# Performance work log

Measured on AMD Instinct MI355X. Metric: run time of the kernel, lower is better.

## Reference

```python
import jax, jax.numpy as jnp
import numpy as np

B, C, H, W = 2, 256, 64, 64
D = 4  # max dilation ring


def _offsets():
    offs = [(0, 0)]
    for s in range(1, D + 1):
        for a in (-s, 0, s):
            for b in (-s, 0, s):
                if a != 0 or b != 0:
                    offs.append((a, b))
    return np.array(offs, dtype=np.int32)  # (33, 2)


def setup_inputs() -> dict:
    key = jax.random.key(0)
    k1, k2, k3, k4 = jax.random.split(key, 4)
    scale = 1.0 / np.sqrt(C)
    return {
        "Ft": jax.random.normal(k1, (B, C, H, W), dtype=jnp.float32),
        "Ft_epsilon": jax.random.normal(k2, (B, C, H, W), dtype=jnp.float32),
        "Wf": jax.random.normal(k3, (256, C), dtype=jnp.float32) * scale,
        "bf": jnp.zeros((256,), dtype=jnp.float32),
        "Wg": jax.random.normal(k4, (256, C), dtype=jnp.float32) * scale,
        "bg": jnp.zeros((256,), dtype=jnp.float32),
    }


def reference(Ft, Ft_epsilon, Wf, bf, Wg, bg):
    # 1x1 conv embeddings
    Ef = jnp.einsum("bchw,oc->bohw", Ft, Wf) + bf[None, :, None, None]          # f(Ft)
    Eg = jnp.einsum("bchw,oc->bohw", Ft_epsilon, Wg) + bg[None, :, None, None]  # g(Ft_eps)

    offs = _offsets()                                  # (K,2), K=33
    dx = jnp.asarray(offs[:, 0])[:, None, None]        # (K,1,1)
    dy = jnp.asarray(offs[:, 1])[:, None, None]
    xs = jnp.arange(H)[None, :, None] + dx             # (K,H,1)
    ys = jnp.arange(W)[None, None, :] + dy             # (K,1,W)
    valid = ((xs >= 0) & (xs < H)) & ((ys >= 0) & (ys < W))  # (K,H,W)
    xc = jnp.clip(xs, 0, H - 1)
    yc = jnp.clip(ys, 0, W - 1)

    # gather neighbor embeddings and features: (B,C,K,H,W)
    Ef_n = Ef[:, :, xc, yc]
    Ft_n = Ft[:, :, xc, yc]

    # affinity of center embedding with each neighbor embedding
    aff = jnp.einsum("bchw,bckhw->bkhw", Eg, Ef_n)     # (B,K,H,W)
    aff = jnp.where(valid[None], aff, -jnp.inf)        # clip out-of-bounds neighbors
    w = jax.nn.softmax(aff, axis=1)                    # (B,K,H,W); center always valid

    out = jnp.einsum("bkhw,bckhw->bchw", w, Ft_n)      # (B,C,H,W)
    return out
```

## Files before the change

kernel.cpp:

```cpp
#include <hip/hip_runtime.h>
#include <math.h>

typedef __attribute__((ext_vector_type(4))) float f4;

__device__ __forceinline__ int iclamp(int x, int lo, int hi) { return min(max(x, lo), hi); }

__device__ constexpr int DXC[33] = {0, -1,-1,-1,0,0,1,1,1, -2,-2,-2,0,0,2,2,2, -3,-3,-3,0,0,3,3,3, -4,-4,-4,0,0,4,4,4};
__device__ constexpr int DYC[33] = {0, -1,0,1,-1,1,-1,0,1, -2,0,2,-2,2,-2,0,2, -3,0,3,-3,3,-3,0,3, -4,0,4,-4,4,-4,0,4};

__global__ __launch_bounds__(256) void mat_M(
    const float* __restrict__ Wf, const float* __restrict__ Wg,
    const float* __restrict__ bg, float* __restrict__ Mt, float* __restrict__ r)
{
    __shared__ float Sf[32][33], Sg[32][33];
    __shared__ float Rs[32][9];
    const int c1b = blockIdx.x * 32, c2b = blockIdx.y * 32;
    const int tid = threadIdx.x;
    const int tx = tid & 15, ty = tid >> 4;
    float acc[2][2] = {};
    for (int ko = 0; ko < 256; ko += 32) {
        #pragma unroll
        for (int i = 0; i < 4; ++i) {
            int f = i * 256 + tid, o = f >> 5, c = f & 31;
            Sf[o][c] = Wf[(ko + o) * 256 + c1b + c];
            Sg[o][c] = Wg[(ko + o) * 256 + c2b + c];
        }
        __syncthreads();
        #pragma unroll
        for (int o = 0; o < 32; ++o) {
            float f0 = Sf[o][ty * 2], f1 = Sf[o][ty * 2 + 1];
            float g0 = Sg[o][tx * 2], g1 = Sg[o][tx * 2 + 1];
            acc[0][0] += f0 * g0; acc[0][1] += f0 * g1;
            acc[1][0] += f1 * g0; acc[1][1] += f1 * g1;
        }
        __syncthreads();
    }
    #pragma unroll
    for (int i = 0; i < 2; ++i)
        #pragma unroll
        for (int j = 0; j < 2; ++j)
            Mt[(size_t)(c2b + tx * 2 + j) * 256 + c1b + ty * 2 + i] = acc[i][j];

    if (blockIdx.y == 0) {
        const int c1l = tid & 31, og = tid >> 5;
        float s = 0.f;
        #pragma unroll 8
        for (int o = og * 32; o < og * 32 + 32; ++o)
            s += Wf[o * 256 + c1b + c1l] * bg[o];
        Rs[c1l][og] = s;
        __syncthreads();
        if (tid < 32) {
            float t = 0.f;
            #pragma unroll
            for (int j = 0; j < 8; ++j) t += Rs[tid][j];
            r[c1b + tid] = t;
        }
    }
}

template<bool LO, bool HI>
__device__ __forceinline__ void ldwin(float* wn, const float* Lb, int rd, int ch, int wq) {
    const float* p = &Lb[(rd * 8 + ch) * 72 + wq * 4];
    if constexpr (LO) { f4 v = *(const f4*)p;       wn[0]=v.x; wn[1]=v.y; wn[2]=v.z;  wn[3]=v.w; }
    {                   f4 v = *(const f4*)(p + 4); wn[4]=v.x; wn[5]=v.y; wn[6]=v.z;  wn[7]=v.w; }
    if constexpr (HI) { f4 v = *(const f4*)(p + 8); wn[8]=v.x; wn[9]=v.y; wn[10]=v.z; wn[11]=v.w; }
}

template<int DY>
__device__ __forceinline__ void fmadd4(f4& a, const f4& eg, const float* wn) {
    a.x += eg.x * wn[4 + DY];
    a.y += eg.y * wn[5 + DY];
    a.z += eg.z * wn[6 + DY];
    a.w += eg.w * wn[7 + DY];
}

template<int KQ>
__device__ __forceinline__ void aff_compute(const float* Lb, const float* egb,
                                            int wq, int cg, f4* acc)
{
    #pragma unroll
    for (int chi = 0; chi < 2; ++chi) {
        const int ch = cg * 2 + chi;
        f4 eg = *(const f4*)&egb[ch * 68 + wq * 4];
        float wn[12];
        if constexpr (KQ == 0) {
            ldwin<true,true>(wn, Lb, 0, ch, wq);
            fmadd4<-4>(acc[0], eg, wn); fmadd4<0>(acc[1], eg, wn); fmadd4<4>(acc[2], eg, wn);
            ldwin<true,true>(wn, Lb, 1, ch, wq);
            fmadd4<-3>(acc[3], eg, wn); fmadd4<0>(acc[4], eg, wn); fmadd4<3>(acc[5], eg, wn);
            ldwin<true,true>(wn, Lb, 2, ch, wq);
            fmadd4<-2>(acc[6], eg, wn); fmadd4<0>(acc[7], eg, wn); fmadd4<2>(acc[8], eg, wn);
        } else if constexpr (KQ == 1) {
            ldwin<true,true>(wn, Lb, 3, ch, wq);
            fmadd4<-1>(acc[0], eg, wn); fmadd4<0>(acc[1], eg, wn); fmadd4<1>(acc[2], eg, wn);
            ldwin<true,false>(wn, Lb, 4, ch, wq);
            fmadd4<-1>(acc[3], eg, wn); fmadd4<-2>(acc[4], eg, wn);
            fmadd4<-3>(acc[5], eg, wn); fmadd4<-4>(acc[6], eg, wn);
        } else if constexpr (KQ == 2) {
            ldwin<false,true>(wn, Lb, 4, ch, wq);
            fmadd4<0>(acc[0], eg, wn); fmadd4<1>(acc[1], eg, wn); fmadd4<2>(acc[2], eg, wn);
            fmadd4<3>(acc[3], eg, wn); fmadd4<4>(acc[4], eg, wn);
            ldwin<true,true>(wn, Lb, 5, ch, wq);
            fmadd4<-1>(acc[5], eg, wn); fmadd4<0>(acc[6], eg, wn); fmadd4<1>(acc[7], eg, wn);
        } else {
            ldwin<true,true>(wn, Lb, 6, ch, wq);
            fmadd4<-2>(acc[0], eg, wn); fmadd4<0>(acc[1], eg, wn); fmadd4<2>(acc[2], eg, wn);
            ldwin<true,true>(wn, Lb, 7, ch, wq);
            fmadd4<-3>(acc[3], eg, wn); fmadd4<0>(acc[4], eg, wn); fmadd4<3>(acc[5], eg, wn);
            ldwin<true,true>(wn, Lb, 8, ch, wq);
            fmadd4<-4>(acc[6], eg, wn); fmadd4<0>(acc[7], eg, wn); fmadd4<4>(acc[8], eg, wn);
        }
    }
}

__global__ __launch_bounds__(256, 2) void gemm_aff(
    const float* __restrict__ Mt, const float* __restrict__ rw,
    const float* __restrict__ FtE, const float* __restrict__ Ftg,
    float* __restrict__ part)
{
    __shared__ float SH[16384];
    const int h = blockIdx.x, b = blockIdx.y, cseg = blockIdx.z;
    const int tid = threadIdx.x;

    float* Gs = SH;
    float* L0 = SH + 4352;

    {
        float* Ms = SH;
        const int tn = tid & 15, tm = tid >> 4;
        const int m0 = cseg * 64;
        const float* X = FtE + (size_t)b * 1048576 + h * 64 + tn * 4;

        #pragma unroll
        for (int i = 0; i < 16; ++i) {
            int f = i * 256 + tid;
            int k = f >> 4, mi = f & 15;
            *(f4*)&Ms[k * 64 + mi * 4] = *(const f4*)&Mt[(size_t)k * 256 + m0 + mi * 4];
        }
        __syncthreads();

        f4 acc0 = {0.f,0.f,0.f,0.f}, acc1 = acc0, acc2 = acc0, acc3 = acc0;
        for (int kc = 0; kc < 256; kc += 8) {
            f4 x0 = *(const f4*)(X + (size_t)(kc + 0) * 4096);
            f4 x1 = *(const f4*)(X + (size_t)(kc + 1) * 4096);
            f4 x2 = *(const f4*)(X + (size_t)(kc + 2) * 4096);
            f4 x3 = *(const f4*)(X + (size_t)(kc + 3) * 4096);
            f4 x4 = *(const f4*)(X + (size_t)(kc + 4) * 4096);
            f4 x5 = *(const f4*)(X + (size_t)(kc + 5) * 4096);
            f4 x6 = *(const f4*)(X + (size_t)(kc + 6) * 4096);
            f4 x7 = *(const f4*)(X + (size_t)(kc + 7) * 4096);
            f4 a0 = *(const f4*)&Ms[(kc + 0) * 64 + tm * 4];
            f4 a1 = *(const f4*)&Ms[(kc + 1) * 64 + tm * 4];
            f4 a2 = *(const f4*)&Ms[(kc + 2) * 64 + tm * 4];
            f4 a3 = *(const f4*)&Ms[(kc + 3) * 64 + tm * 4];
            f4 a4 = *(const f4*)&Ms[(kc + 4) * 64 + tm * 4];
            f4 a5 = *(const f4*)&Ms[(kc + 5) * 64 + tm * 4];
            f4 a6 = *(const f4*)&Ms[(kc + 6) * 64 + tm * 4];
            f4 a7 = *(const f4*)&Ms[(kc + 7) * 64 + tm * 4];
            acc0 += x0 * a0.x; acc1 += x0 * a0.y; acc2 += x0 * a0.z; acc3 += x0 * a0.w;
            acc0 += x1 * a1.x; acc1 += x1 * a1.y; acc2 += x1 * a1.z; acc3 += x1 * a1.w;
            acc0 += x2 * a2.x; acc1 += x2 * a2.y; acc2 += x2 * a2.z; acc3 += x2 * a2.w;
            acc0 += x3 * a3.x; acc1 += x3 * a3.y; acc2 += x3 * a3.z; acc3 += x3 * a3.w;
            acc0 += x4 * a4.x; acc1 += x4 * a4.y; acc2 += x4 * a4.z; acc3 += x4 * a4.w;
            acc0 += x5 * a5.x; acc1 += x5 * a5.y; acc2 += x5 * a5.z; acc3 += x5 * a5.w;
            acc0 += x6 * a6.x; acc1 += x6 * a6.y; acc2 += x6 * a6.z; acc3 += x6 * a6.w;
            acc0 += x7 * a7.x; acc1 += x7 * a7.y; acc2 += x7 * a7.z; acc3 += x7 * a7.w;
        }
        __syncthreads();

        const int m0g = m0 + tm * 4;
        f4 v;
        v = acc0 + rw[m0g + 0]; *(f4*)&Gs[(tm * 4 + 0) * 68 + tn * 4] = v;
        v = acc1 + rw[m0g + 1]; *(f4*)&Gs[(tm * 4 + 1) * 68 + tn * 4] = v;
        v = acc2 + rw[m0g + 2]; *(f4*)&Gs[(tm * 4 + 2) * 68 + tn * 4] = v;
        v = acc3 + rw[m0g + 3]; *(f4*)&Gs[(tm * 4 + 3) * 68 + tn * 4] = v;
    }

    const int wq = tid & 15, cg = (tid >> 4) & 3, kq = tid >> 6;
    const float* FtB = Ftg + (size_t)b * 1048576;
    const int cbase = cseg * 64;

    int hr[9];
    #pragma unroll
    for (int d = 0; d < 9; ++d) hr[d] = iclamp(h + d - 4, 0, 63);

    f4 vreg[5]; float sreg[3];

    auto load_rnd = [&](int rr) {
        const int c0 = cbase + rr * 8;
        #pragma unroll
        for (int i = 0; i < 5; ++i) {
            int f = i * 256 + tid;
            if (f < 1152) {
                int d = f >> 7, rem = f & 127, ch = rem >> 4, c4 = rem & 15;
                vreg[i] = *(const f4*)&FtB[(size_t)(c0 + ch) * 4096 + hr[d] * 64 + c4 * 4];
            }
        }
        #pragma unroll
        for (int i = 0; i < 3; ++i) {
            int e = i * 256 + tid;
            if (e < 576) {
                int row = e >> 3, sc = e & 7, d = row >> 3, ch = row & 7;
                int wsrc = (sc < 4) ? 0 : 63;
                sreg[i] = FtB[(size_t)(c0 + ch) * 4096 + hr[d] * 64 + wsrc];
            }
        }
    };
    auto store_rnd = [&](int buf) {
        float* Lb = L0 + buf * 5184;
        #pragma unroll
        for (int i = 0; i < 5; ++i) {
            int f = i * 256 + tid;
            if (f < 1152) {
                int d = f >> 7, rem = f & 127, ch = rem >> 4, c4 = rem & 15;
                *(f4*)&Lb[(d * 8 + ch) * 72 + 4 + c4 * 4] = vreg[i];
            }
        }
        #pragma unroll
        for (int i = 0; i < 3; ++i) {
            int e = i * 256 + tid;
            if (e < 576) {
                int row = e >> 3, sc = e & 7, d = row >> 3, ch = row & 7;
                int col = (sc < 4) ? sc : (64 + sc);
                Lb[(d * 8 + ch) * 72 + col] = sreg[i];
            }
        }
    };

    f4 acc[9] = {};

    load_rnd(0); store_rnd(0);
    for (int rr = 0; rr < 8; ++rr) {
        if (rr < 7) load_rnd(rr + 1);
        __syncthreads();
        const float* Lb = L0 + (rr & 1) * 5184;
        const float* egb = Gs + rr * 8 * 68;
        switch (kq) {
            case 0: aff_compute<0>(Lb, egb, wq, cg, acc); break;
            case 1: aff_compute<1>(Lb, egb, wq, cg, acc); break;
            case 2: aff_compute<2>(Lb, egb, wq, cg, acc); break;
            default: aff_compute<3>(Lb, egb, wq, cg, acc); break;
        }
        if (rr < 7) store_rnd((rr + 1) & 1);
    }

    #pragma unroll
    for (int j = 0; j < 9; ++j) {
        acc[j].x += __shfl_xor(acc[j].x, 16); acc[j].x += __shfl_xor(acc[j].x, 32);
        acc[j].y += __shfl_xor(acc[j].y, 16); acc[j].y += __shfl_xor(acc[j].y, 32);
        acc[j].z += __shfl_xor(acc[j].z, 16); acc[j].z += __shfl_xor(acc[j].z, 32);
        acc[j].w += __shfl_xor(acc[j].w, 16); acc[j].w += __shfl_xor(acc[j].w, 32);
    }

    if (cg == 0) {
        float* pB = part + (((size_t)cseg * 2 + b) * 33) * 4096 + h * 64 + wq * 4;
        #define STP(K, J) *(f4*)&pB[(size_t)(K) * 4096] = acc[J];
        switch (kq) {
            case 0: STP(25,0) STP(26,1) STP(27,2) STP(17,3) STP(18,4) STP(19,5) STP(9,6) STP(10,7) STP(11,8) break;
            case 1: STP(1,0) STP(2,1) STP(3,2) STP(4,3) STP(12,4) STP(20,5) STP(28,6) break;
            case 2: STP(0,0) STP(5,1) STP(13,2) STP(21,3) STP(29,4) STP(6,5) STP(7,6) STP(8,7) break;
            default: STP(14,0) STP(15,1) STP(16,2) STP(22,3) STP(23,4) STP(24,5) STP(30,6) STP(31,7) STP(32,8) break;
        }
        #undef STP
    }
}

__global__ __launch_bounds__(256, 2) void out_kernel(
    const float* __restrict__ part, const float* __restrict__ Ft,
    float* __restrict__ out)
{
    __shared__ float L[2][9 * 8 * 72];

    const int h = blockIdx.x, b = blockIdx.y, cseg = blockIdx.z;
    const int tid = threadIdx.x;
    const int w = tid & 63, cg = tid >> 6;
    const size_t plane = (size_t)b * 256 * 4096;
    const float* FtB = Ft + plane;
    float* outB = out + plane;
    const int cbase = cseg * 64;
    const int p = h * 64 + w;

    int hr[9];
    #pragma unroll
    for (int d = 0; d < 9; ++d) hr[d] = iclamp(h + d - 4, 0, 63);

    f4 vreg[5]; float sreg[3];

    auto load_rnd = [&](int rr) {
        const int c0 = cbase + rr * 8;
        #pragma unroll
        for (int i = 0; i < 5; ++i) {
            int f = i * 256 + tid;
            if (f < 1152) {
                int d = f >> 7, rem = f & 127, ch = rem >> 4, c4 = rem & 15;
                vreg[i] = *(const f4*)&FtB[(size_t)(c0 + ch) * 4096 + hr[d] * 64 + c4 * 4];
            }
        }
        #pragma unroll
        for (int i = 0; i < 3; ++i) {
            int e = i * 256 + tid;
            if (e < 576) {
                int row = e >> 3, sc = e & 7, d = row >> 3, ch = row & 7;
                int wsrc = (sc < 4) ? 0 : 63;
                sreg[i] = FtB[(size_t)(c0 + ch) * 4096 + hr[d] * 64 + wsrc];
            }
        }
    };
    auto store_rnd = [&](int buf) {
        float* Lb = L[buf];
        #pragma unroll
        for (int i = 0; i < 5; ++i) {
            int f = i * 256 + tid;
            if (f < 1152) {
                int d = f >> 7, rem = f & 127, ch = rem >> 4, c4 = rem & 15;
                *(f4*)&Lb[(d * 8 + ch) * 72 + 4 + c4 * 4] = vreg[i];
            }
        }
        #pragma unroll
        for (int i = 0; i < 3; ++i) {
            int e = i * 256 + tid;
            if (e < 576) {
                int row = e >> 3, sc = e & 7, d = row >> 3, ch = row & 7;
                int col = (sc < 4) ? sc : (64 + sc);
                Lb[(d * 8 + ch) * 72 + col] = sreg[i];
            }
        }
    };

    load_rnd(0);

    float wv[33];
    {
        constexpr size_t CS = (size_t)2 * 33 * 4096;
        const float* pB = part + ((size_t)b * 33) * 4096 + p;
        float mx = -INFINITY;
        #pragma unroll
        for (int k = 0; k < 33; ++k) {
            size_t off = (size_t)k * 4096;
            float s = pB[off] + pB[CS + off] + pB[2 * CS + off] + pB[3 * CS + off];
            bool valid = ((unsigned)(h + DXC[k]) < 64u) && ((unsigned)(w + DYC[k]) < 64u);
            wv[k] = valid ? s : -INFINITY;
            mx = fmaxf(mx, wv[k]);
        }
        float ssum = 0.f;
        #pragma unroll
        for (int k = 0; k < 33; ++k) { float e = __expf(wv[k] - mx); wv[k] = e; ssum += e; }
        float inv = 1.0f / ssum;
        #pragma unroll
        for (int k = 0; k < 33; ++k) wv[k] *= inv;
    }

    store_rnd(0);
    for (int rr = 0; rr < 8; ++rr) {
        if (rr < 7) load_rnd(rr + 1);
        __syncthreads();
        const float* base = &L[rr & 1][4 + w];
        #pragma unroll
        for (int u = 0; u < 2; ++u) {
            const float* b2 = base + (cg * 2 + u) * 72;
            float o = 0.f;
            #pragma unroll
            for (int k = 0; k < 33; ++k)
                o += wv[k] * b2[(DXC[k] + 4) * 576 + DYC[k]];
            int c = cbase + rr * 8 + cg * 2 + u;
            outB[(size_t)c * 4096 + p] = o;
        }
        if (rr < 7) store_rnd((rr + 1) & 1);
    }
}

extern "C" void kernel_launch(void* const* d_in, const int* in_sizes, int n_in,
                              void* d_out, int out_size, void* d_ws, size_t ws_size,
                              hipStream_t stream) {
    const float* Ft  = (const float*)d_in[0];
    const float* FtE = (const float*)d_in[1];
    const float* Wf  = (const float*)d_in[2];
    const float* bf  = (const float*)d_in[3];
    const float* Wg  = (const float*)d_in[4];
    const float* bg  = (const float*)d_in[5];
    float* out = (float*)d_out;
    (void)bf;

    float* part = (float*)d_ws;
    float* Mt   = part + (size_t)4 * 2 * 33 * 4096;
    float* rw   = Mt + 256 * 256;

    hipLaunchKernelGGL(mat_M,      dim3(8, 8),     dim3(256), 0, stream, Wf, Wg, bg, Mt, rw);
    hipLaunchKernelGGL(gemm_aff,   dim3(64, 2, 4), dim3(256), 0, stream, Mt, rw, FtE, Ft, part);
    hipLaunchKernelGGL(out_kernel, dim3(64, 2, 4), dim3(256), 0, stream, part, Ft, out);
}
```

Baseline: 141.2 us.

## Split out_kernel neighbor sum across offset groups with vectorized window loads

The output aggregation is restructured so each thread handles four adjacent pixels and one quarter of the 33 offsets (grouped by row), reusing a loaded 12-wide LDS window across several offsets. Softmax weights are staged through shared memory and redistributed per offset group. The four partial sums are reduced through an extra shared buffer, then stored with float4 writes. This cuts LDS reads per FMA but adds a __syncthreads, extra shared memory, and only half the threads do the final reduction and store.

```diff
diff --git a/kernel.cpp b/kernel.cpp
--- a/kernel.cpp
+++ b/kernel.cpp
@@ -265,15 +265,60 @@
     }
 }
 
+template<int KQ>
+__device__ __forceinline__ void out_compute(const float* Lb, const f4* wv,
+                                            int wq, int ch0, f4* acc)
+{
+    #pragma unroll
+    for (int chi = 0; chi < 2; ++chi) {
+        const int ch = ch0 + chi;
+        f4& a = acc[chi];
+        float wn[12];
+        if constexpr (KQ == 0) {
+            ldwin<true,true>(wn, Lb, 0, ch, wq);
+            fmadd4<-4>(a, wv[0], wn); fmadd4<0>(a, wv[1], wn); fmadd4<4>(a, wv[2], wn);
+            ldwin<true,true>(wn, Lb, 1, ch, wq);
+            fmadd4<-3>(a, wv[3], wn); fmadd4<0>(a, wv[4], wn); fmadd4<3>(a, wv[5], wn);
+            ldwin<true,true>(wn, Lb, 2, ch, wq);
+            fmadd4<-2>(a, wv[6], wn); fmadd4<0>(a, wv[7], wn); fmadd4<2>(a, wv[8], wn);
+        } else if constexpr (KQ == 1) {
+            ldwin<true,true>(wn, Lb, 3, ch, wq);
+            fmadd4<-1>(a, wv[0], wn); fmadd4<0>(a, wv[1], wn); fmadd4<1>(a, wv[2], wn);
+            ldwin<true,false>(wn, Lb, 4, ch, wq);
+            fmadd4<-1>(a, wv[3], wn); fmadd4<-2>(a, wv[4], wn);
+            fmadd4<-3>(a, wv[5], wn); fmadd4<-4>(a, wv[6], wn);
+        } else if constexpr (KQ == 2) {
+            ldwin<false,true>(wn, Lb, 4, ch, wq);
+            fmadd4<0>(a, wv[0], wn); fmadd4<1>(a, wv[1], wn); fmadd4<2>(a, wv[2], wn);
+            fmadd4<3>(a, wv[3], wn); fmadd4<4>(a, wv[4], wn);
+            ldwin<true,true>(wn, Lb, 5, ch, wq);
+            fmadd4<-1>(a, wv[5], wn); fmadd4<0>(a, wv[6], wn); fmadd4<1>(a, wv[7], wn);
+        } else {
+            ldwin<true,true>(wn, Lb, 6, ch, wq);
+            fmadd4<-2>(a, wv[0], wn); fmadd4<0>(a, wv[1], wn); fmadd4<2>(a, wv[2], wn);
+            ldwin<true,true>(wn, Lb, 7, ch, wq);
+            fmadd4<-3>(a, wv[3], wn); fmadd4<0>(a, wv[4], wn); fmadd4<3>(a, wv[5], wn);
+            ldwin<true,true>(wn, Lb, 8, ch, wq);
+            fmadd4<-4>(a, wv[6], wn); fmadd4<0>(a, wv[7], wn); fmadd4<4>(a, wv[8], wn);
+        }
+    }
+}
+
+__device__ constexpr int KGQ[33] = {2, 1,1,1,1, 2, 2,2,2, 0,0,0, 1, 2, 3,3,3, 0,0,0, 1, 2, 3,3,3, 0,0,0, 1, 2, 3,3,3};
+__device__ constexpr int KJX[33] = {0, 0,1,2,3, 1, 5,6,7, 6,7,8, 4, 2, 0,1,2, 3,4,5, 5, 3, 3,4,5, 0,1,2, 6, 4, 6,7,8};
+
 __global__ __launch_bounds__(256, 2) void out_kernel(
     const float* __restrict__ part, const float* __restrict__ Ft,
     float* __restrict__ out)
 {
     __shared__ float L[2][9 * 8 * 72];
+    __shared__ float WG[33 * 64];
+    __shared__ float PL[4][8 * 68];
 
     const int h = blockIdx.x, b = blockIdx.y, cseg = blockIdx.z;
     const int tid = threadIdx.x;
-    const int w = tid & 63, cg = tid >> 6;
+    const int w = tid & 63;
+    const int wq = tid & 15, cg = (tid >> 4) & 3, kq = tid >> 6;
     const size_t plane = (size_t)b * 256 * 4096;
     const float* FtB = Ft + plane;
     float* outB = out + plane;
@@ -329,8 +374,8 @@
 
     load_rnd(0);
 
-    float wv[33];
     {
+        float wv[33];
         constexpr size_t CS = (size_t)2 * 33 * 4096;
         const float* pB = part + ((size_t)b * 33) * 4096 + p;
         float mx = -INFINITY;
@@ -347,23 +392,42 @@
         for (int k = 0; k < 33; ++k) { float e = __expf(wv[k] - mx); wv[k] = e; ssum += e; }
         float inv = 1.0f / ssum;
         #pragma unroll
-        for (int k = 0; k < 33; ++k) wv[k] *= inv;
+        for (int k = 0; k < 33; ++k) {
+            int wk = (k < 9) ? 0 : (k < 17) ? 1 : (k < 25) ? 2 : 3;
+            if (kq == wk) WG[k * 64 + w] = wv[k] * inv;
+        }
     }
 
     store_rnd(0);
+    __syncthreads();
+
+    f4 wv4[9] = {};
+    #pragma unroll
+    for (int k = 0; k < 33; ++k)
+        if (kq == KGQ[k]) wv4[KJX[k]] = *(const f4*)&WG[k * 64 + wq * 4];
+
     for (int rr = 0; rr < 8; ++rr) {
         if (rr < 7) load_rnd(rr + 1);
-        __syncthreads();
-        const float* base = &L[rr & 1][4 + w];
-        #pragma unroll
-        for (int u = 0; u < 2; ++u) {
-            const float* b2 = base + (cg * 2 + u) * 72;
-            float o = 0.f;
-            #pragma unroll
-            for (int k = 0; k < 33; ++k)
-                o += wv[k] * b2[(DXC[k] + 4) * 576 + DYC[k]];
-            int c = cbase + rr * 8 + cg * 2 + u;
-            outB[(size_t)c * 4096 + p] = o;
+        if (rr > 0) __syncthreads();
+        const float* Lb = L[rr & 1];
+        f4 acc[2] = {};
+        switch (kq) {
+            case 0: out_compute<0>(Lb, wv4, wq, cg * 2, acc); break;
+            case 1: out_compute<1>(Lb, wv4, wq, cg * 2, acc); break;
+            case 2: out_compute<2>(Lb, wv4, wq, cg * 2, acc); break;
+            default: out_compute<3>(Lb, wv4, wq, cg * 2, acc); break;
+        }
+        *(f4*)&PL[kq][(cg * 2 + 0) * 68 + wq * 4] = acc[0];
+        *(f4*)&PL[kq][(cg * 2 + 1) * 68 + wq * 4] = acc[1];
+        __syncthreads();
+        if (tid < 128) {
+            int ch = tid >> 4, ws = tid & 15;
+            f4 s = *(const f4*)&PL[0][ch * 68 + ws * 4];
+            s += *(const f4*)&PL[1][ch * 68 + ws * 4];
+            s += *(const f4*)&PL[2][ch * 68 + ws * 4];
+            s += *(const f4*)&PL[3][ch * 68 + ws * 4];
+            int c = cbase + rr * 8 + ch;
+            *(f4*)&outB[(size_t)c * 4096 + h * 64 + ws * 4] = s;
         }
         if (rr < 7) store_rnd((rr + 1) & 1);
     }
```

Measured after the change: 142.7 us. No clear change (+1.1%).
